# Kernel optimization log

Hardware: AMD Instinct MI355X
Metric: run time of the kernel (lower is better)

## Reference

```python
import jax, jax.numpy as jnp
import numpy as np

BS, N1, N2, D = 2, 512, 512, 64  # in_dim = out_dim = D
TEMP = 1.0
EPS = 1e-5
POOL_RATIO = 0.5


def setup_inputs() -> dict:
    key = jax.random.key(0)
    ks = iter(jax.random.split(key, 32))
    nrm = lambda shape, s=0.05: jax.random.normal(next(ks), shape, dtype=jnp.float32) * s
    inp = {
        "x1": jax.random.normal(next(ks), (BS, N1, D), dtype=jnp.float32),
        "x2": jax.random.normal(next(ks), (BS, N2, D), dtype=jnp.float32),
        # proj_type1 / proj_type2 (Linear in->in); weights stored [in, out]
        "W1": nrm((D, D)), "b1": jnp.zeros((D,), jnp.float32),
        "W2": nrm((D, D)), "b2": jnp.zeros((D,), jnp.float32),
        # att_proj / att_projM (Linear in->out)
        "Wa": nrm((D, D)), "ba": jnp.zeros((D,), jnp.float32),
        "WaM": nrm((D, D)), "baM": jnp.zeros((D,), jnp.float32),
        # attention weight vectors (out_dim, 1)
        "w11": nrm((D, 1), 0.2), "w22": nrm((D, 1), 0.2),
        "w12": nrm((D, 1), 0.2), "wM": nrm((D, 1), 0.2),
        # projections
        "Wpa": nrm((D, D)), "bpa": jnp.zeros((D,), jnp.float32),
        "Wwoa": nrm((D, D)), "bwoa": jnp.zeros((D,), jnp.float32),
        "WpaM": nrm((D, D)), "bpaM": jnp.zeros((D,), jnp.float32),
        "WwoaM": nrm((D, D)), "bwoaM": jnp.zeros((D,), jnp.float32),
        # BatchNorm1d affine params
        "gamma": jnp.ones((D,), jnp.float32), "beta": jnp.zeros((D,), jnp.float32),
        # GraphPool score layer (Linear D->1), shared pool as in Model
        "Wp": nrm((D, 1), 0.2), "bp": jnp.zeros((1,), jnp.float32),
    }
    return inp


def _htrg_gat(x1, x2, W1, b1, W2, b2, Wa, ba, WaM, baM, w11, w22, w12, wM,
              Wpa, bpa, Wwoa, bwoa, WpaM, bpaM, WwoaM, bwoaM, gamma, beta):
    n1 = x1.shape[1]
    x1p = x1 @ W1 + b1
    x2p = x2 @ W2 + b2
    x = jnp.concatenate([x1p, x2p], axis=1)          # (b, N, d)
    master = jnp.mean(x, axis=1, keepdims=True)       # (b, 1, d)

    # --- attention map: pairwise node products, blockwise score weights ---
    pair = x[:, :, None, :] * x[:, None, :, :]        # (b, N, N, d)
    t = jnp.tanh(pair @ Wa + ba)                      # (b, N, N, d)
    top = jnp.concatenate([t[:, :n1, :n1] @ w11, t[:, :n1, n1:] @ w12], axis=2)
    bot = jnp.concatenate([t[:, n1:, :n1] @ w12, t[:, n1:, n1:] @ w22], axis=2)
    board = jnp.concatenate([top, bot], axis=1) / TEMP  # (b, N, N, 1)
    att = jax.nn.softmax(board, axis=-2)

    # --- master update ---
    tm = jnp.tanh((x * master) @ WaM + baM)           # (b, N, d)
    am = jax.nn.softmax((tm @ wM) / TEMP, axis=-2)    # (b, N, 1)
    agg_m = jnp.einsum('bn,bnd->bd', am[..., 0], x)[:, None, :]  # (b, 1, d)
    master_new = (agg_m @ WpaM + bpaM) + (master @ WwoaM + bwoaM)

    # --- project nodes with attention ---
    agg = jnp.einsum('bij,bjd->bid', att[..., 0], x)  # (b, N, d)
    xo = (agg @ Wpa + bpa) + (x @ Wwoa + bwoa)

    # --- BatchNorm1d over flattened (b*N) rows, then SELU ---
    mu = jnp.mean(xo, axis=(0, 1))
    var = jnp.var(xo, axis=(0, 1))
    xo = (xo - mu) * jax.lax.rsqrt(var + EPS) * gamma + beta
    xo = jax.nn.selu(xo)
    return xo[:, :n1], xo[:, n1:], master_new


def _graph_pool(x, Wp, bp):
    # scores -> sigmoid -> scale features -> top-k gather
    n = x.shape[1]
    k = max(int(n * POOL_RATIO), 1)
    scores = jax.nn.sigmoid(x @ Wp + bp)              # (b, n, 1)
    _, idx = jax.lax.top_k(scores[..., 0], k)         # (b, k)
    xs = x * scores
    return jnp.take_along_axis(xs, idx[..., None], axis=1)  # (b, k, d)


def reference(x1, x2, W1, b1, W2, b2, Wa, ba, WaM, baM, w11, w22, w12, wM,
              Wpa, bpa, Wwoa, bwoa, WpaM, bpaM, WwoaM, bwoaM, gamma, beta, Wp, bp):
    o1, o2, master = _htrg_gat(x1, x2, W1, b1, W2, b2, Wa, ba, WaM, baM,
                               w11, w22, w12, wM, Wpa, bpa, Wwoa, bwoa,
                               WpaM, bpaM, WwoaM, bwoaM, gamma, beta)
    p1 = _graph_pool(o1, Wp, bp)
    p2 = _graph_pool(o2, Wp, bp)
    return jnp.concatenate([p1, p2], axis=1)          # (b, n1/2 + n2/2, d)
```

## Files before the change

### kernel.cpp

```cpp
#include <hip/hip_runtime.h>

typedef float f32x4 __attribute__((ext_vector_type(4)));
typedef short short8 __attribute__((ext_vector_type(8)));

#define N_TOT 1024
#define N_HALF 512
#define D 64
#define KPOOL 256

#if __has_builtin(__builtin_amdgcn_exp2f)
#define EXP2F(x) __builtin_amdgcn_exp2f(x)
#else
#define EXP2F(x) __expf((x) * 0.6931471805599453f)
#endif
#if __has_builtin(__builtin_amdgcn_rcpf)
#define RCPF(x) __builtin_amdgcn_rcpf(x)
#else
#define RCPF(x) (1.0f / (x))
#endif

__device__ __forceinline__ short f2bf(float v) {
    unsigned u = __float_as_uint(v);
    u += 0x7FFFu + ((u >> 16) & 1u);
    return (short)(u >> 16);
}
__device__ __forceinline__ float bf2f(unsigned short u) {
    return __uint_as_float(((unsigned)u) << 16);
}

__global__ void k_proj(const float* __restrict__ x1, const float* __restrict__ x2,
                       const float* __restrict__ W1, const float* __restrict__ b1,
                       const float* __restrict__ W2, const float* __restrict__ b2,
                       float* __restrict__ x_f, unsigned short* __restrict__ x_bf,
                       unsigned short* __restrict__ xT_hi, unsigned short* __restrict__ xT_lo) {
    int r = blockIdx.x;
    int b = r >> 10, n = r & 1023;
    const float *src, *W, *bias;
    if (n < N_HALF) { src = x1 + (b * N_HALF + n) * D;            W = W1; bias = b1; }
    else            { src = x2 + (b * N_HALF + (n - N_HALF)) * D; W = W2; bias = b2; }
    __shared__ float row[D];
    int t = threadIdx.x;
    row[t] = src[t];
    __syncthreads();
    float acc = bias[t];
#pragma unroll
    for (int d = 0; d < D; ++d) acc = fmaf(row[d], W[d * D + t], acc);
    unsigned short hi = (unsigned short)f2bf(acc);
    unsigned short lo = (unsigned short)f2bf(acc - bf2f(hi));
    x_f[r * D + t] = acc;
    x_bf[r * D + t] = hi;
    xT_hi[((size_t)b * D + t) * N_TOT + n] = hi;
    xT_lo[((size_t)b * D + t) * N_TOT + n] = lo;
}

__global__ void __launch_bounds__(256)
k_score(const float* __restrict__ x_f, const unsigned short* __restrict__ x_bf,
        const float* __restrict__ Wa, const float* __restrict__ ba,
        const float* __restrict__ w11, const float* __restrict__ w22,
        const float* __restrict__ w12,
        unsigned short* __restrict__ Ehi, unsigned short* __restrict__ Elo) {
    int bid = blockIdx.x;
    int b = (bid >= 2560) ? 1 : 0;
    int m = bid - b * 2560;
    int i, c0;
    if (m < 1024)      { i = m >> 2;                        c0 = m & 3; }
    else if (m < 1792) { int t = m - 1024; i = 256 + t / 3; c0 = t % 3; }
    else if (m < 2304) { int t = m - 1792; i = 512 + (t >> 1); c0 = t & 1; }
    else               { i = 768 + (m - 2304);              c0 = 0; }
    int jt0 = i >> 4;
    int jts = jt0 + (c0 << 4);
    int jte = (jts + 16 < 64) ? (jts + 16) : 64;

    int tid = threadIdx.x;
    int l = tid & 63, wv = tid >> 6;
    int kc = l & 15, dg = l >> 4;

    __shared__ float xi_s[D];
    if (tid < D) xi_s[tid] = x_f[(b * N_TOT + i) * D + tid];
    __syncthreads();

    const float C2 = 2.885390081777927f;
    const float LOG2E = 1.4426950408889634f;

    const float* wTop = (i < N_HALF) ? w11 : w12;
    const float* wBot = (i < N_HALF) ? w12 : w22;

    short8 bfrag[4][2];
    float bac[4], wm2A[4], wm2B[4];
    float wsumA = 0.f, wsumB = 0.f;
#pragma unroll
    for (int kt = 0; kt < 4; ++kt) {
        int kcol = kt * 16 + kc;
        bac[kt] = ba[kcol] * C2;
        float wA = wTop[kcol], wB = wBot[kcol];
        wm2A[kt] = -2.f * wA; wm2B[kt] = -2.f * wB;
        wsumA += wA; wsumB += wB;
#pragma unroll
        for (int mm = 0; mm < 2; ++mm) {
            short8 f;
#pragma unroll
            for (int e = 0; e < 8; ++e) {
                int d = mm * 32 + dg * 8 + e;
                f[e] = f2bf(xi_s[d] * Wa[d * D + kcol]);
            }
            bfrag[kt][mm] = f;
        }
    }

    const unsigned short* xb_b = x_bf + b * N_TOT * D;
    unsigned short* EbH = Ehi + ((size_t)b << 20);
    unsigned short* EbL = Elo + ((size_t)b << 20);
    for (int jt = jts + wv; jt < jte; jt += 4) {
        const unsigned short* arow = xb_b + (jt * 16 + kc) * D + dg * 8;
        short8 a0 = *reinterpret_cast<const short8*>(arow);
        short8 a1 = *reinterpret_cast<const short8*>(arow + 32);
        f32x4 acc[4];
#pragma unroll
        for (int kt = 0; kt < 4; ++kt) {
            f32x4 z = {0.f, 0.f, 0.f, 0.f};
            z = __builtin_amdgcn_mfma_f32_16x16x32_bf16(a0, bfrag[kt][0], z, 0, 0, 0);
            z = __builtin_amdgcn_mfma_f32_16x16x32_bf16(a1, bfrag[kt][1], z, 0, 0, 0);
            acc[kt] = z;
        }
        bool top = (jt < 32);
        float wsum_t = top ? wsumA : wsumB;
#pragma unroll
        for (int r = 0; r < 4; ++r) {
            float part = wsum_t;
#pragma unroll
            for (int kt = 0; kt < 4; ++kt) {
                float e2 = EXP2F(fmaf(acc[kt][r], C2, bac[kt]));
                float rcv = RCPF(e2 + 1.f);
                part = fmaf(top ? wm2A[kt] : wm2B[kt], rcv, part);
            }
            part += __shfl_xor(part, 1);
            part += __shfl_xor(part, 2);
            part += __shfl_xor(part, 4);
            part += __shfl_xor(part, 8);
            if (kc == 0) {
                int j = jt * 16 + dg * 4 + r;
                if (j >= i) {
                    float e = EXP2F(part * LOG2E);
                    unsigned short eh = (unsigned short)f2bf(e);
                    unsigned short el = (unsigned short)f2bf(e - bf2f(eh));
                    EbH[(size_t)i * N_TOT + j] = eh;
                    EbL[(size_t)i * N_TOT + j] = el;
                    if (j > i) {
                        EbH[(size_t)j * N_TOT + i] = eh;
                        EbL[(size_t)j * N_TOT + i] = el;
                    }
                }
            }
        }
    }
}

__global__ void __launch_bounds__(256)
k_agg(const unsigned short* __restrict__ Ehi, const unsigned short* __restrict__ Elo,
      const unsigned short* __restrict__ xT_hi, const unsigned short* __restrict__ xT_lo,
      const float* __restrict__ x_f,
      const float* __restrict__ Wpa, const float* __restrict__ bpa,
      const float* __restrict__ Wwoa, const float* __restrict__ bwoa,
      float* __restrict__ xo_pre, float* __restrict__ partials) {
    int b = blockIdx.x >> 6, it = blockIdx.x & 63;
    int i0 = it * 16;
    int tid = threadIdx.x;
    int l = tid & 63, wv = tid >> 6;
    int kc = l & 15, dg = l >> 4;

    const unsigned short* EbH = Ehi + ((size_t)b << 20);
    const unsigned short* EbL = Elo + ((size_t)b << 20);
    const unsigned short* xTH = xT_hi + (size_t)b * D * N_TOT;
    const unsigned short* xTL = xT_lo + (size_t)b * D * N_TOT;

    f32x4 C0 = {0.f, 0.f, 0.f, 0.f}, C1 = C0, C2v = C0;
    const unsigned short* AH = EbH + (size_t)(i0 + kc) * N_TOT + dg * 8;
    const unsigned short* AL = EbL + (size_t)(i0 + kc) * N_TOT + dg * 8;
    const unsigned short* BH = xTH + (size_t)(wv * 16 + kc) * N_TOT + dg * 8;
    const unsigned short* BL = xTL + (size_t)(wv * 16 + kc) * N_TOT + dg * 8;
#pragma unroll 4
    for (int ks = 0; ks < 32; ++ks) {
        short8 ah = *reinterpret_cast<const short8*>(AH + ks * 32);
        short8 bh = *reinterpret_cast<const short8*>(BH + ks * 32);
        C0 = __builtin_amdgcn_mfma_f32_16x16x32_bf16(ah, bh, C0, 0, 0, 0);
        short8 bl = *reinterpret_cast<const short8*>(BL + ks * 32);
        C1 = __builtin_amdgcn_mfma_f32_16x16x32_bf16(ah, bl, C1, 0, 0, 0);
        short8 al = *reinterpret_cast<const short8*>(AL + ks * 32);
        C2v = __builtin_amdgcn_mfma_f32_16x16x32_bf16(al, bh, C2v, 0, 0, 0);
    }
    f32x4 C = (C0 + C1) + C2v;

    __shared__ float aggL[16][D];
    __shared__ float xiL[16][D];
    __shared__ float xoL[16][D];
    __shared__ float rs_part[4][16];
    __shared__ float riL[16];

    {
        int row = l & 15, seg = l >> 4;
        size_t base = (size_t)(i0 + row) * N_TOT + wv * 256 + seg * 64;
        const unsigned short* ErH = EbH + base;
        const unsigned short* ErL = EbL + base;
        float rs = 0.f;
#pragma unroll
        for (int u = 0; u < 8; ++u) {
            short8 vh = *reinterpret_cast<const short8*>(ErH + u * 8);
            short8 vl = *reinterpret_cast<const short8*>(ErL + u * 8);
#pragma unroll
            for (int e = 0; e < 8; ++e)
                rs += bf2f((unsigned short)vh[e]) + bf2f((unsigned short)vl[e]);
        }
        rs += __shfl_xor(rs, 16);
        rs += __shfl_xor(rs, 32);
        if (l < 16) rs_part[wv][l] = rs;
    }

#pragma unroll
    for (int r = 0; r < 4; ++r)
        aggL[dg * 4 + r][wv * 16 + kc] = C[r];

    {
        int row = tid >> 4, quad = tid & 15;
        const f32x4* xf4 = reinterpret_cast<const f32x4*>(x_f + ((size_t)b * N_TOT + i0) * D);
        reinterpret_cast<f32x4*>(xiL)[row * 16 + quad] = xf4[row * 16 + quad];
    }
    __syncthreads();
    if (tid < 16)
        riL[tid] = 1.f / (rs_part[0][tid] + rs_part[1][tid] + rs_part[2][tid] + rs_part[3][tid]);
    __syncthreads();
#pragma unroll
    for (int u = 0; u < 4; ++u) {
        int idx = tid + 256 * u;
        reinterpret_cast<float*>(aggL)[idx] *= riL[idx >> 6];
    }
    __syncthreads();

    int k = l;
    float xo[4];
#pragma unroll
    for (int r = 0; r < 4; ++r) xo[r] = bpa[k] + bwoa[k];
    for (int dd = 0; dd < D; ++dd) {
        float wp = Wpa[dd * D + k], ww = Wwoa[dd * D + k];
#pragma unroll
        for (int r = 0; r < 4; ++r) {
            int row = wv * 4 + r;
            xo[r] += aggL[row][dd] * wp + xiL[row][dd] * ww;
        }
    }
#pragma unroll
    for (int r = 0; r < 4; ++r) {
        int row = wv * 4 + r;
        xo_pre[((size_t)b * N_TOT + i0 + row) * D + k] = xo[r];
        xoL[row][k] = xo[r];
    }
    __syncthreads();
    if (tid < D) {
        float s = 0.f, q = 0.f;
#pragma unroll
        for (int mm = 0; mm < 16; ++mm) { float v = xoL[mm][tid]; s += v; q = fmaf(v, v, q); }
        partials[blockIdx.x * 128 + tid] = s;
        partials[blockIdx.x * 128 + 64 + tid] = q;
    }
}

__global__ void k_stats2(const float* __restrict__ partials, float* __restrict__ stats) {
    int t = threadIdx.x;
    int g = t >> 7;
    int f128 = t & 127;
    float s = 0.f;
    for (int blk = g * 32; blk < g * 32 + 32; ++blk) s += partials[blk * 128 + f128];
    __shared__ float SQ[4][128];
    SQ[g][f128] = s;
    __syncthreads();
    if (t < 128) {
        float tot = SQ[0][t] + SQ[1][t] + SQ[2][t] + SQ[3][t];
        SQ[0][t] = tot;
    }
    __syncthreads();
    if (t < D) {
        float mu = SQ[0][t] * (1.f / 2048.f);
        float ex2 = SQ[0][64 + t] * (1.f / 2048.f);
        stats[t] = mu;
        stats[D + t] = rsqrtf(ex2 - mu * mu + 1e-5f);
    }
}

__global__ void k_norm(const float* __restrict__ xo_pre, const float* __restrict__ stats,
                       const float* __restrict__ gamma, const float* __restrict__ beta,
                       const float* __restrict__ Wp, const float* __restrict__ bp,
                       float* __restrict__ o_norm, float* __restrict__ scores) {
    int r = blockIdx.x * 4 + (threadIdx.x >> 6);
    int t = threadIdx.x & 63;
    float v = xo_pre[r * D + t];
    v = (v - stats[t]) * stats[D + t] * gamma[t] + beta[t];
    const float kScale = 1.0507009873554805f, kAlpha = 1.6732632423543772f;
    v = (v > 0.f) ? kScale * v : kScale * kAlpha * expm1f(v);
    o_norm[r * D + t] = v;
    float pd = v * Wp[t];
#pragma unroll
    for (int off = 32; off >= 1; off >>= 1) pd += __shfl_xor(pd, off);
    if (t == 0) scores[r] = 1.f / (1.f + __expf(-(pd + bp[0])));
}

__global__ void __launch_bounds__(512)
k_pool(const float* __restrict__ o_norm, const float* __restrict__ scores,
       float* __restrict__ out) {
    int b = blockIdx.x >> 1, half = blockIdx.x & 1;
    int tid = threadIdx.x;
    __shared__ float sc_s[N_HALF];
    __shared__ unsigned long long keys[N_HALF];
    __shared__ unsigned short map[KPOOL];

    {
        float sc = scores[b * N_TOT + half * N_HALF + tid];
        sc_s[tid] = sc;
        keys[tid] = ((unsigned long long)__float_as_uint(sc) << 10) | (unsigned)(511 - tid);
    }
    __syncthreads();
    unsigned long long mine = keys[tid];
    int cnt = 0;
#pragma unroll 8
    for (int qq = 0; qq < N_HALF; ++qq) cnt += (keys[qq] > mine) ? 1 : 0;
    if (cnt < KPOOL) map[cnt] = (unsigned short)tid;
    __syncthreads();
    int d = tid & 63;
    for (int rr = tid >> 6; rr < KPOOL; rr += 8) {
        int src = map[rr];
        out[(size_t)(b * N_HALF + half * KPOOL + rr) * D + d] =
            o_norm[(size_t)(b * N_TOT + half * N_HALF + src) * D + d] * sc_s[src];
    }
}

extern "C" void kernel_launch(void* const* d_in, const int* in_sizes, int n_in,
                              void* d_out, int out_size, void* d_ws, size_t ws_size,
                              hipStream_t stream) {
    const float* x1   = (const float*)d_in[0];
    const float* x2   = (const float*)d_in[1];
    const float* W1   = (const float*)d_in[2];
    const float* b1   = (const float*)d_in[3];
    const float* W2   = (const float*)d_in[4];
    const float* b2   = (const float*)d_in[5];
    const float* Wa   = (const float*)d_in[6];
    const float* ba   = (const float*)d_in[7];
    const float* w11  = (const float*)d_in[10];
    const float* w22  = (const float*)d_in[11];
    const float* w12  = (const float*)d_in[12];
    const float* Wpa  = (const float*)d_in[14];
    const float* bpa  = (const float*)d_in[15];
    const float* Wwoa = (const float*)d_in[16];
    const float* bwoa = (const float*)d_in[17];
    const float* gamma= (const float*)d_in[22];
    const float* beta = (const float*)d_in[23];
    const float* Wp   = (const float*)d_in[24];
    const float* bp   = (const float*)d_in[25];
    float* out = (float*)d_out;

    char* ws = (char*)d_ws;
    float*          x_f     = (float*)(ws + 0);
    unsigned short* x_bf    = (unsigned short*)(ws + 524288);
    unsigned short* xT_hi   = (unsigned short*)(ws + 786432);
    unsigned short* xT_lo   = (unsigned short*)(ws + 1048576);
    unsigned short* Ehi     = (unsigned short*)(ws + 1310720);
    unsigned short* Elo     = (unsigned short*)(ws + 5505024);
    float*          xo_pre  = (float*)(ws + 9699328);
    float*          o_norm  = (float*)(ws + 10223616);
    float*          scores  = (float*)(ws + 10747904);
    float*          partials= (float*)(ws + 10756096);
    float*          stats   = (float*)(ws + 10821632);

    hipLaunchKernelGGL(k_proj, dim3(2 * N_TOT), dim3(64), 0, stream,
                       x1, x2, W1, b1, W2, b2, x_f, x_bf, xT_hi, xT_lo);
    hipLaunchKernelGGL(k_score, dim3(5120), dim3(256), 0, stream,
                       x_f, x_bf, Wa, ba, w11, w22, w12, Ehi, Elo);
    hipLaunchKernelGGL(k_agg, dim3(128), dim3(256), 0, stream,
                       Ehi, Elo, xT_hi, xT_lo, x_f, Wpa, bpa, Wwoa, bwoa, xo_pre, partials);
    hipLaunchKernelGGL(k_stats2, dim3(1), dim3(512), 0, stream, partials, stats);
    hipLaunchKernelGGL(k_norm, dim3(512), dim3(256), 0, stream,
                       xo_pre, stats, gamma, beta, Wp, bp, o_norm, scores);
    hipLaunchKernelGGL(k_pool, dim3(4), dim3(512), 0, stream, o_norm, scores, out);
}
```

Before: 103.5 us.

## Split aggregation over key quarters and stage transposed Wa for score kernel

The aggregation kernel, previously 128 blocks each doing the full 1024-long reduction, is split into 512 blocks that each handle a quarter of the key dimension. They write partial aggregates and row sums, and a new finalize kernel reduces them and applies the output projections and BN partial statistics. The change is meant to fix poor GPU occupancy in the aggregation stage. It costs an extra kernel launch and a round trip of partial results through global memory. Separately, Wa is transposed once in an extra k_proj block so that k_score can load weights and bias/score vectors as vectors or through shared memory instead of strided scalar global loads.

```diff
diff --git a/kernel.cpp b/kernel.cpp
--- a/kernel.cpp
+++ b/kernel.cpp
@@ -31,15 +31,20 @@
 __global__ void k_proj(const float* __restrict__ x1, const float* __restrict__ x2,
                        const float* __restrict__ W1, const float* __restrict__ b1,
                        const float* __restrict__ W2, const float* __restrict__ b2,
+                       const float* __restrict__ Wa, float* __restrict__ WaT_f,
                        float* __restrict__ x_f, unsigned short* __restrict__ x_bf,
                        unsigned short* __restrict__ xT_hi, unsigned short* __restrict__ xT_lo) {
+    int t = threadIdx.x;
+    if (blockIdx.x == 2048) {
+        for (int k = 0; k < D; ++k) WaT_f[k * D + t] = Wa[t * D + k];
+        return;
+    }
     int r = blockIdx.x;
     int b = r >> 10, n = r & 1023;
     const float *src, *W, *bias;
     if (n < N_HALF) { src = x1 + (b * N_HALF + n) * D;            W = W1; bias = b1; }
     else            { src = x2 + (b * N_HALF + (n - N_HALF)) * D; W = W2; bias = b2; }
     __shared__ float row[D];
-    int t = threadIdx.x;
     row[t] = src[t];
     __syncthreads();
     float acc = bias[t];
@@ -55,7 +60,7 @@
 
 __global__ void __launch_bounds__(256)
 k_score(const float* __restrict__ x_f, const unsigned short* __restrict__ x_bf,
-        const float* __restrict__ Wa, const float* __restrict__ ba,
+        const float* __restrict__ WaT_f, const float* __restrict__ ba,
         const float* __restrict__ w11, const float* __restrict__ w22,
         const float* __restrict__ w12,
         unsigned short* __restrict__ Ehi, unsigned short* __restrict__ Elo) {
@@ -75,34 +80,42 @@
     int l = tid & 63, wv = tid >> 6;
     int kc = l & 15, dg = l >> 4;
 
-    __shared__ float xi_s[D];
-    if (tid < D) xi_s[tid] = x_f[(b * N_TOT + i) * D + tid];
-    __syncthreads();
-
     const float C2 = 2.885390081777927f;
     const float LOG2E = 1.4426950408889634f;
 
     const float* wTop = (i < N_HALF) ? w11 : w12;
     const float* wBot = (i < N_HALF) ? w12 : w22;
+
+    __shared__ float xi_s[D];
+    __shared__ float ba_s[D], wA_s[D], wB_s[D];
+    if (tid < D) xi_s[tid] = x_f[(b * N_TOT + i) * D + tid];
+    else if (tid < 2 * D) ba_s[tid - D] = ba[tid - D] * C2;
+    else if (tid < 3 * D) wA_s[tid - 2 * D] = wTop[tid - 2 * D];
+    else                  wB_s[tid - 3 * D] = wBot[tid - 3 * D];
+    __syncthreads();
 
     short8 bfrag[4][2];
     float bac[4], wm2A[4], wm2B[4];
     float wsumA = 0.f, wsumB = 0.f;
+    const f32x4* xi4 = reinterpret_cast<const f32x4*>(xi_s);
 #pragma unroll
     for (int kt = 0; kt < 4; ++kt) {
         int kcol = kt * 16 + kc;
-        bac[kt] = ba[kcol] * C2;
-        float wA = wTop[kcol], wB = wBot[kcol];
+        bac[kt] = ba_s[kcol];
+        float wA = wA_s[kcol], wB = wB_s[kcol];
         wm2A[kt] = -2.f * wA; wm2B[kt] = -2.f * wB;
         wsumA += wA; wsumB += wB;
+        const float* wrow = WaT_f + kcol * D;
 #pragma unroll
         for (int mm = 0; mm < 2; ++mm) {
+            const f32x4* wp = reinterpret_cast<const f32x4*>(wrow + mm * 32 + dg * 8);
+            f32x4 w0 = wp[0], w1 = wp[1];
+            f32x4 xa = xi4[mm * 8 + dg * 2], xb = xi4[mm * 8 + dg * 2 + 1];
             short8 f;
 #pragma unroll
-            for (int e = 0; e < 8; ++e) {
-                int d = mm * 32 + dg * 8 + e;
-                f[e] = f2bf(xi_s[d] * Wa[d * D + kcol]);
-            }
+            for (int e = 0; e < 4; ++e) f[e] = f2bf(xa[e] * w0[e]);
+#pragma unroll
+            for (int e = 0; e < 4; ++e) f[e + 4] = f2bf(xb[e] * w1[e]);
             bfrag[kt][mm] = f;
         }
     }
@@ -156,14 +169,13 @@
 }
 
 __global__ void __launch_bounds__(256)
-k_agg(const unsigned short* __restrict__ Ehi, const unsigned short* __restrict__ Elo,
-      const unsigned short* __restrict__ xT_hi, const unsigned short* __restrict__ xT_lo,
-      const float* __restrict__ x_f,
-      const float* __restrict__ Wpa, const float* __restrict__ bpa,
-      const float* __restrict__ Wwoa, const float* __restrict__ bwoa,
-      float* __restrict__ xo_pre, float* __restrict__ partials) {
-    int b = blockIdx.x >> 6, it = blockIdx.x & 63;
-    int i0 = it * 16;
+k_aggp(const unsigned short* __restrict__ Ehi, const unsigned short* __restrict__ Elo,
+       const unsigned short* __restrict__ xT_hi, const unsigned short* __restrict__ xT_lo,
+       float* __restrict__ pagg, float* __restrict__ rowsum_part) {
+    int blk = blockIdx.x;
+    int b = blk >> 8, rest = blk & 255;
+    int it = rest >> 2, q = rest & 3;
+    int i0 = it * 16, jbase = q * 256;
     int tid = threadIdx.x;
     int l = tid & 63, wv = tid >> 6;
     int kc = l & 15, dg = l >> 4;
@@ -174,12 +186,12 @@
     const unsigned short* xTL = xT_lo + (size_t)b * D * N_TOT;
 
     f32x4 C0 = {0.f, 0.f, 0.f, 0.f}, C1 = C0, C2v = C0;
-    const unsigned short* AH = EbH + (size_t)(i0 + kc) * N_TOT + dg * 8;
-    const unsigned short* AL = EbL + (size_t)(i0 + kc) * N_TOT + dg * 8;
-    const unsigned short* BH = xTH + (size_t)(wv * 16 + kc) * N_TOT + dg * 8;
-    const unsigned short* BL = xTL + (size_t)(wv * 16 + kc) * N_TOT + dg * 8;
-#pragma unroll 4
-    for (int ks = 0; ks < 32; ++ks) {
+    const unsigned short* AH = EbH + (size_t)(i0 + kc) * N_TOT + jbase + dg * 8;
+    const unsigned short* AL = EbL + (size_t)(i0 + kc) * N_TOT + jbase + dg * 8;
+    const unsigned short* BH = xTH + (size_t)(wv * 16 + kc) * N_TOT + jbase + dg * 8;
+    const unsigned short* BL = xTL + (size_t)(wv * 16 + kc) * N_TOT + jbase + dg * 8;
+#pragma unroll
+    for (int ks = 0; ks < 8; ++ks) {
         short8 ah = *reinterpret_cast<const short8*>(AH + ks * 32);
         short8 bh = *reinterpret_cast<const short8*>(BH + ks * 32);
         C0 = __builtin_amdgcn_mfma_f32_16x16x32_bf16(ah, bh, C0, 0, 0, 0);
@@ -190,76 +202,70 @@
     }
     f32x4 C = (C0 + C1) + C2v;
 
-    __shared__ float aggL[16][D];
-    __shared__ float xiL[16][D];
-    __shared__ float xoL[16][D];
-    __shared__ float rs_part[4][16];
-    __shared__ float riL[16];
-
     {
-        int row = l & 15, seg = l >> 4;
-        size_t base = (size_t)(i0 + row) * N_TOT + wv * 256 + seg * 64;
-        const unsigned short* ErH = EbH + base;
-        const unsigned short* ErL = EbL + base;
+        int row = wv * 4 + (l & 3);
+        int seg = l >> 2;
+        size_t base = (size_t)(i0 + row) * N_TOT + jbase + seg * 16;
         float rs = 0.f;
 #pragma unroll
-        for (int u = 0; u < 8; ++u) {
-            short8 vh = *reinterpret_cast<const short8*>(ErH + u * 8);
-            short8 vl = *reinterpret_cast<const short8*>(ErL + u * 8);
+        for (int u = 0; u < 2; ++u) {
+            short8 vh = *reinterpret_cast<const short8*>(EbH + base + u * 8);
+            short8 vl = *reinterpret_cast<const short8*>(EbL + base + u * 8);
 #pragma unroll
             for (int e = 0; e < 8; ++e)
                 rs += bf2f((unsigned short)vh[e]) + bf2f((unsigned short)vl[e]);
         }
+        rs += __shfl_xor(rs, 4);
+        rs += __shfl_xor(rs, 8);
         rs += __shfl_xor(rs, 16);
         rs += __shfl_xor(rs, 32);
-        if (l < 16) rs_part[wv][l] = rs;
+        if (l < 4) rowsum_part[(size_t)(b * 4 + q) * N_TOT + i0 + wv * 4 + l] = rs;
     }
 
 #pragma unroll
     for (int r = 0; r < 4; ++r)
-        aggL[dg * 4 + r][wv * 16 + kc] = C[r];
-
-    {
-        int row = tid >> 4, quad = tid & 15;
-        const f32x4* xf4 = reinterpret_cast<const f32x4*>(x_f + ((size_t)b * N_TOT + i0) * D);
-        reinterpret_cast<f32x4*>(xiL)[row * 16 + quad] = xf4[row * 16 + quad];
-    }
-    __syncthreads();
-    if (tid < 16)
-        riL[tid] = 1.f / (rs_part[0][tid] + rs_part[1][tid] + rs_part[2][tid] + rs_part[3][tid]);
-    __syncthreads();
-#pragma unroll
-    for (int u = 0; u < 4; ++u) {
-        int idx = tid + 256 * u;
-        reinterpret_cast<float*>(aggL)[idx] *= riL[idx >> 6];
-    }
-    __syncthreads();
-
-    int k = l;
-    float xo[4];
-#pragma unroll
-    for (int r = 0; r < 4; ++r) xo[r] = bpa[k] + bwoa[k];
-    for (int dd = 0; dd < D; ++dd) {
-        float wp = Wpa[dd * D + k], ww = Wwoa[dd * D + k];
-#pragma unroll
-        for (int r = 0; r < 4; ++r) {
-            int row = wv * 4 + r;
-            xo[r] += aggL[row][dd] * wp + xiL[row][dd] * ww;
-        }
-    }
-#pragma unroll
-    for (int r = 0; r < 4; ++r) {
-        int row = wv * 4 + r;
-        xo_pre[((size_t)b * N_TOT + i0 + row) * D + k] = xo[r];
-        xoL[row][k] = xo[r];
-    }
-    __syncthreads();
-    if (tid < D) {
-        float s = 0.f, q = 0.f;
-#pragma unroll
-        for (int mm = 0; mm < 16; ++mm) { float v = xoL[mm][tid]; s += v; q = fmaf(v, v, q); }
-        partials[blockIdx.x * 128 + tid] = s;
-        partials[blockIdx.x * 128 + 64 + tid] = q;
+        pagg[((size_t)(b * 4 + q) * N_TOT + i0 + dg * 4 + r) * D + wv * 16 + kc] = C[r];
+}
+
+__global__ void __launch_bounds__(256)
+k_aggfin(const float* __restrict__ pagg, const float* __restrict__ rowsum_part,
+         const float* __restrict__ x_f,
+         const float* __restrict__ Wpa, const float* __restrict__ bpa,
+         const float* __restrict__ Wwoa, const float* __restrict__ bwoa,
+         float* __restrict__ xo_pre, float* __restrict__ partials) {
+    int tid = threadIdx.x;
+    int rl = tid >> 6, k = tid & 63;
+    int r = blockIdx.x * 4 + rl;
+    int b = r >> 10, i = r & 1023;
+
+    float rs = 0.f, a = 0.f;
+#pragma unroll
+    for (int jc = 0; jc < 4; ++jc) {
+        rs += rowsum_part[(size_t)(b * 4 + jc) * N_TOT + i];
+        a  += pagg[((size_t)(b * 4 + jc) * N_TOT + i) * D + k];
+    }
+    float ri = 1.f / rs;
+
+    __shared__ float aggL[4][D];
+    __shared__ float xiL[4][D];
+    aggL[rl][k] = a * ri;
+    xiL[rl][k] = x_f[(size_t)r * D + k];
+    __syncthreads();
+    float xo = bpa[k] + bwoa[k];
+#pragma unroll 8
+    for (int dd = 0; dd < D; ++dd)
+        xo += aggL[rl][dd] * Wpa[dd * D + k] + xiL[rl][dd] * Wwoa[dd * D + k];
+    xo_pre[(size_t)r * D + k] = xo;
+
+    __syncthreads();
+    aggL[rl][k] = xo;
+    xiL[rl][k] = xo * xo;
+    __syncthreads();
+    if (rl == 0) {
+        float s = aggL[0][k] + aggL[1][k] + aggL[2][k] + aggL[3][k];
+        float qs = xiL[0][k] + xiL[1][k] + xiL[2][k] + xiL[3][k];
+        partials[blockIdx.x * 128 + k] = s;
+        partials[blockIdx.x * 128 + 64 + k] = qs;
     }
 }
 
@@ -268,7 +274,7 @@
     int g = t >> 7;
     int f128 = t & 127;
     float s = 0.f;
-    for (int blk = g * 32; blk < g * 32 + 32; ++blk) s += partials[blk * 128 + f128];
+    for (int blk = g * 128; blk < g * 128 + 128; ++blk) s += partials[blk * 128 + f128];
     __shared__ float SQ[4][128];
     SQ[g][f128] = s;
     __syncthreads();
@@ -362,18 +368,23 @@
     unsigned short* xT_lo   = (unsigned short*)(ws + 1048576);
     unsigned short* Ehi     = (unsigned short*)(ws + 1310720);
     unsigned short* Elo     = (unsigned short*)(ws + 5505024);
-    float*          xo_pre  = (float*)(ws + 9699328);
-    float*          o_norm  = (float*)(ws + 10223616);
-    float*          scores  = (float*)(ws + 10747904);
-    float*          partials= (float*)(ws + 10756096);
-    float*          stats   = (float*)(ws + 10821632);
-
-    hipLaunchKernelGGL(k_proj, dim3(2 * N_TOT), dim3(64), 0, stream,
-                       x1, x2, W1, b1, W2, b2, x_f, x_bf, xT_hi, xT_lo);
+    float*          WaT_f   = (float*)(ws + 9699328);
+    float*          pagg    = (float*)(ws + 9715712);
+    float*          rowsum  = (float*)(ws + 11812864);
+    float*          xo_pre  = (float*)(ws + 11845632);
+    float*          o_norm  = (float*)(ws + 12369920);
+    float*          scores  = (float*)(ws + 12894208);
+    float*          partials= (float*)(ws + 12902400);
+    float*          stats   = (float*)(ws + 13164544);
+
+    hipLaunchKernelGGL(k_proj, dim3(2 * N_TOT + 1), dim3(64), 0, stream,
+                       x1, x2, W1, b1, W2, b2, Wa, WaT_f, x_f, x_bf, xT_hi, xT_lo);
     hipLaunchKernelGGL(k_score, dim3(5120), dim3(256), 0, stream,
-                       x_f, x_bf, Wa, ba, w11, w22, w12, Ehi, Elo);
-    hipLaunchKernelGGL(k_agg, dim3(128), dim3(256), 0, stream,
-                       Ehi, Elo, xT_hi, xT_lo, x_f, Wpa, bpa, Wwoa, bwoa, xo_pre, partials);
+                       x_f, x_bf, WaT_f, ba, w11, w22, w12, Ehi, Elo);
+    hipLaunchKernelGGL(k_aggp, dim3(512), dim3(256), 0, stream,
+                       Ehi, Elo, xT_hi, xT_lo, pagg, rowsum);
+    hipLaunchKernelGGL(k_aggfin, dim3(512), dim3(256), 0, stream,
+                       pagg, rowsum, x_f, Wpa, bpa, Wwoa, bwoa, xo_pre, partials);
     hipLaunchKernelGGL(k_stats2, dim3(1), dim3(512), 0, stream, partials, stats);
     hipLaunchKernelGGL(k_norm, dim3(512), dim3(256), 0, stream,
                        xo_pre, stats, gamma, beta, Wp, bp, o_norm, scores);
```

Measured after the change: 144.5 us. 1.4x slower.

## Pack hi/lo attention weights and split aggregation over key halves

Applied to the files above, without the earlier changes.

Stores the hi and lo bf16 halves of each attention weight packed into one 32-bit word, so the score kernel issues one store per element instead of two and the aggregation reads one stream. The aggregation kernel is split into a partial kernel over two halves of the key dimension, doubling the grid from 128 to 256 blocks, and a finalize kernel that sums the partials and applies the projections. This adds an extra launch and an fp32 partial-buffer round trip in exchange for more parallelism in the memory-bound reduction.

```diff
diff --git a/kernel.cpp b/kernel.cpp
--- a/kernel.cpp
+++ b/kernel.cpp
@@ -57,8 +57,7 @@
 k_score(const float* __restrict__ x_f, const unsigned short* __restrict__ x_bf,
         const float* __restrict__ Wa, const float* __restrict__ ba,
         const float* __restrict__ w11, const float* __restrict__ w22,
-        const float* __restrict__ w12,
-        unsigned short* __restrict__ Ehi, unsigned short* __restrict__ Elo) {
+        const float* __restrict__ w12, unsigned* __restrict__ Ep) {
     int bid = blockIdx.x;
     int b = (bid >= 2560) ? 1 : 0;
     int m = bid - b * 2560;
@@ -108,8 +107,7 @@
     }
 
     const unsigned short* xb_b = x_bf + b * N_TOT * D;
-    unsigned short* EbH = Ehi + ((size_t)b << 20);
-    unsigned short* EbL = Elo + ((size_t)b << 20);
+    unsigned* Eb = Ep + ((size_t)b << 20);
     for (int jt = jts + wv; jt < jte; jt += 4) {
         const unsigned short* arow = xb_b + (jt * 16 + kc) * D + dg * 8;
         short8 a0 = *reinterpret_cast<const short8*>(arow);
@@ -143,12 +141,9 @@
                     float e = EXP2F(part * LOG2E);
                     unsigned short eh = (unsigned short)f2bf(e);
                     unsigned short el = (unsigned short)f2bf(e - bf2f(eh));
-                    EbH[(size_t)i * N_TOT + j] = eh;
-                    EbL[(size_t)i * N_TOT + j] = el;
-                    if (j > i) {
-                        EbH[(size_t)j * N_TOT + i] = eh;
-                        EbL[(size_t)j * N_TOT + i] = el;
-                    }
+                    unsigned pk = ((unsigned)eh << 16) | (unsigned)el;
+                    Eb[(size_t)i * N_TOT + j] = pk;
+                    if (j > i) Eb[(size_t)j * N_TOT + i] = pk;
                 }
             }
         }
@@ -156,81 +151,105 @@
 }
 
 __global__ void __launch_bounds__(256)
-k_agg(const unsigned short* __restrict__ Ehi, const unsigned short* __restrict__ Elo,
-      const unsigned short* __restrict__ xT_hi, const unsigned short* __restrict__ xT_lo,
-      const float* __restrict__ x_f,
-      const float* __restrict__ Wpa, const float* __restrict__ bpa,
-      const float* __restrict__ Wwoa, const float* __restrict__ bwoa,
-      float* __restrict__ xo_pre, float* __restrict__ partials) {
+k_aggp(const unsigned* __restrict__ Ep,
+       const unsigned short* __restrict__ xT_hi, const unsigned short* __restrict__ xT_lo,
+       float* __restrict__ pagg, float* __restrict__ rowsum_part) {
+    int blk = blockIdx.x;
+    int b = blk >> 7, rest = blk & 127;
+    int it = rest >> 1, jh = rest & 1;
+    int i0 = it * 16, jbase = jh * 512;
+    int tid = threadIdx.x;
+    int l = tid & 63, wv = tid >> 6;
+    int kc = l & 15, dg = l >> 4;
+
+    const unsigned* Eb = Ep + ((size_t)b << 20);
+    const unsigned short* xTH = xT_hi + (size_t)b * D * N_TOT;
+    const unsigned short* xTL = xT_lo + (size_t)b * D * N_TOT;
+
+    f32x4 C0 = {0.f, 0.f, 0.f, 0.f}, C1 = C0, C2v = C0;
+    const unsigned* Ap = Eb + (size_t)(i0 + kc) * N_TOT + jbase + dg * 8;
+    const unsigned short* BH = xTH + (size_t)(wv * 16 + kc) * N_TOT + jbase + dg * 8;
+    const unsigned short* BL = xTL + (size_t)(wv * 16 + kc) * N_TOT + jbase + dg * 8;
+#pragma unroll 4
+    for (int ks = 0; ks < 16; ++ks) {
+        uint4 p0 = *reinterpret_cast<const uint4*>(Ap + ks * 32);
+        uint4 p1 = *reinterpret_cast<const uint4*>(Ap + ks * 32 + 4);
+        short8 ah, al;
+        ah[0] = (short)(p0.x >> 16); al[0] = (short)(p0.x & 0xffff);
+        ah[1] = (short)(p0.y >> 16); al[1] = (short)(p0.y & 0xffff);
+        ah[2] = (short)(p0.z >> 16); al[2] = (short)(p0.z & 0xffff);
+        ah[3] = (short)(p0.w >> 16); al[3] = (short)(p0.w & 0xffff);
+        ah[4] = (short)(p1.x >> 16); al[4] = (short)(p1.x & 0xffff);
+        ah[5] = (short)(p1.y >> 16); al[5] = (short)(p1.y & 0xffff);
+        ah[6] = (short)(p1.z >> 16); al[6] = (short)(p1.z & 0xffff);
+        ah[7] = (short)(p1.w >> 16); al[7] = (short)(p1.w & 0xffff);
+        short8 bh = *reinterpret_cast<const short8*>(BH + ks * 32);
+        short8 bl = *reinterpret_cast<const short8*>(BL + ks * 32);
+        C0 = __builtin_amdgcn_mfma_f32_16x16x32_bf16(ah, bh, C0, 0, 0, 0);
+        C1 = __builtin_amdgcn_mfma_f32_16x16x32_bf16(ah, bl, C1, 0, 0, 0);
+        C2v = __builtin_amdgcn_mfma_f32_16x16x32_bf16(al, bh, C2v, 0, 0, 0);
+    }
+    f32x4 C = (C0 + C1) + C2v;
+
+    {
+        int row = wv * 4 + (l & 3);
+        int seg = l >> 2;
+        const unsigned* Er = Eb + (size_t)(i0 + row) * N_TOT + jbase + seg * 32;
+        float rs = 0.f;
+#pragma unroll
+        for (int u = 0; u < 8; ++u) {
+            uint4 v = *reinterpret_cast<const uint4*>(Er + u * 4);
+            rs += __uint_as_float(v.x & 0xffff0000u) + __uint_as_float(v.x << 16);
+            rs += __uint_as_float(v.y & 0xffff0000u) + __uint_as_float(v.y << 16);
+            rs += __uint_as_float(v.z & 0xffff0000u) + __uint_as_float(v.z << 16);
+            rs += __uint_as_float(v.w & 0xffff0000u) + __uint_as_float(v.w << 16);
+        }
+        rs += __shfl_xor(rs, 4);
+        rs += __shfl_xor(rs, 8);
+        rs += __shfl_xor(rs, 16);
+        rs += __shfl_xor(rs, 32);
+        if ((l & 3) == (l >> 2) % 4 && l < 4)
+            ;
+        if (l < 4) rowsum_part[(size_t)(b * 2 + jh) * N_TOT + i0 + wv * 4 + l] = rs;
+    }
+
+#pragma unroll
+    for (int r = 0; r < 4; ++r)
+        pagg[((size_t)(b * 2 + jh) * N_TOT + i0 + dg * 4 + r) * D + wv * 16 + kc] = C[r];
+}
+
+__global__ void __launch_bounds__(256)
+k_aggfin(const float* __restrict__ pagg, const float* __restrict__ rowsum_part,
+         const float* __restrict__ x_f,
+         const float* __restrict__ Wpa, const float* __restrict__ bpa,
+         const float* __restrict__ Wwoa, const float* __restrict__ bwoa,
+         float* __restrict__ xo_pre, float* __restrict__ partials) {
     int b = blockIdx.x >> 6, it = blockIdx.x & 63;
     int i0 = it * 16;
     int tid = threadIdx.x;
     int l = tid & 63, wv = tid >> 6;
-    int kc = l & 15, dg = l >> 4;
-
-    const unsigned short* EbH = Ehi + ((size_t)b << 20);
-    const unsigned short* EbL = Elo + ((size_t)b << 20);
-    const unsigned short* xTH = xT_hi + (size_t)b * D * N_TOT;
-    const unsigned short* xTL = xT_lo + (size_t)b * D * N_TOT;
-
-    f32x4 C0 = {0.f, 0.f, 0.f, 0.f}, C1 = C0, C2v = C0;
-    const unsigned short* AH = EbH + (size_t)(i0 + kc) * N_TOT + dg * 8;
-    const unsigned short* AL = EbL + (size_t)(i0 + kc) * N_TOT + dg * 8;
-    const unsigned short* BH = xTH + (size_t)(wv * 16 + kc) * N_TOT + dg * 8;
-    const unsigned short* BL = xTL + (size_t)(wv * 16 + kc) * N_TOT + dg * 8;
-#pragma unroll 4
-    for (int ks = 0; ks < 32; ++ks) {
-        short8 ah = *reinterpret_cast<const short8*>(AH + ks * 32);
-        short8 bh = *reinterpret_cast<const short8*>(BH + ks * 32);
-        C0 = __builtin_amdgcn_mfma_f32_16x16x32_bf16(ah, bh, C0, 0, 0, 0);
-        short8 bl = *reinterpret_cast<const short8*>(BL + ks * 32);
-        C1 = __builtin_amdgcn_mfma_f32_16x16x32_bf16(ah, bl, C1, 0, 0, 0);
-        short8 al = *reinterpret_cast<const short8*>(AL + ks * 32);
-        C2v = __builtin_amdgcn_mfma_f32_16x16x32_bf16(al, bh, C2v, 0, 0, 0);
-    }
-    f32x4 C = (C0 + C1) + C2v;
 
     __shared__ float aggL[16][D];
     __shared__ float xiL[16][D];
     __shared__ float xoL[16][D];
-    __shared__ float rs_part[4][16];
     __shared__ float riL[16];
 
-    {
-        int row = l & 15, seg = l >> 4;
-        size_t base = (size_t)(i0 + row) * N_TOT + wv * 256 + seg * 64;
-        const unsigned short* ErH = EbH + base;
-        const unsigned short* ErL = EbL + base;
-        float rs = 0.f;
-#pragma unroll
-        for (int u = 0; u < 8; ++u) {
-            short8 vh = *reinterpret_cast<const short8*>(ErH + u * 8);
-            short8 vl = *reinterpret_cast<const short8*>(ErL + u * 8);
-#pragma unroll
-            for (int e = 0; e < 8; ++e)
-                rs += bf2f((unsigned short)vh[e]) + bf2f((unsigned short)vl[e]);
-        }
-        rs += __shfl_xor(rs, 16);
-        rs += __shfl_xor(rs, 32);
-        if (l < 16) rs_part[wv][l] = rs;
-    }
-
-#pragma unroll
-    for (int r = 0; r < 4; ++r)
-        aggL[dg * 4 + r][wv * 16 + kc] = C[r];
-
-    {
-        int row = tid >> 4, quad = tid & 15;
-        const f32x4* xf4 = reinterpret_cast<const f32x4*>(x_f + ((size_t)b * N_TOT + i0) * D);
-        reinterpret_cast<f32x4*>(xiL)[row * 16 + quad] = xf4[row * 16 + quad];
-    }
-    __syncthreads();
+    const float* p0 = pagg + ((size_t)(b * 2 + 0) * N_TOT + i0) * D;
+    const float* p1 = pagg + ((size_t)(b * 2 + 1) * N_TOT + i0) * D;
+    const float* xB = x_f + ((size_t)b * N_TOT + i0) * D;
+#pragma unroll
+    for (int u = 0; u < 4; ++u) {
+        int idx = tid + u * 256;
+        reinterpret_cast<float*>(aggL)[idx] = p0[idx] + p1[idx];
+        reinterpret_cast<float*>(xiL)[idx] = xB[idx];
+    }
     if (tid < 16)
-        riL[tid] = 1.f / (rs_part[0][tid] + rs_part[1][tid] + rs_part[2][tid] + rs_part[3][tid]);
+        riL[tid] = 1.f / (rowsum_part[(size_t)(b * 2 + 0) * N_TOT + i0 + tid] +
+                          rowsum_part[(size_t)(b * 2 + 1) * N_TOT + i0 + tid]);
     __syncthreads();
 #pragma unroll
     for (int u = 0; u < 4; ++u) {
-        int idx = tid + 256 * u;
+        int idx = tid + u * 256;
         reinterpret_cast<float*>(aggL)[idx] *= riL[idx >> 6];
     }
     __syncthreads();
@@ -360,20 +379,23 @@
     unsigned short* x_bf    = (unsigned short*)(ws + 524288);
     unsigned short* xT_hi   = (unsigned short*)(ws + 786432);
     unsigned short* xT_lo   = (unsigned short*)(ws + 1048576);
-    unsigned short* Ehi     = (unsigned short*)(ws + 1310720);
-    unsigned short* Elo     = (unsigned short*)(ws + 5505024);
-    float*          xo_pre  = (float*)(ws + 9699328);
-    float*          o_norm  = (float*)(ws + 10223616);
-    float*          scores  = (float*)(ws + 10747904);
-    float*          partials= (float*)(ws + 10756096);
-    float*          stats   = (float*)(ws + 10821632);
+    unsigned*       Ep      = (unsigned*)(ws + 1310720);
+    float*          pagg    = (float*)(ws + 9699328);
+    float*          rowsum  = (float*)(ws + 10747904);
+    float*          xo_pre  = (float*)(ws + 10764288);
+    float*          o_norm  = (float*)(ws + 11288576);
+    float*          scores  = (float*)(ws + 11812864);
+    float*          partials= (float*)(ws + 11821056);
+    float*          stats   = (float*)(ws + 11886592);
 
     hipLaunchKernelGGL(k_proj, dim3(2 * N_TOT), dim3(64), 0, stream,
                        x1, x2, W1, b1, W2, b2, x_f, x_bf, xT_hi, xT_lo);
     hipLaunchKernelGGL(k_score, dim3(5120), dim3(256), 0, stream,
-                       x_f, x_bf, Wa, ba, w11, w22, w12, Ehi, Elo);
-    hipLaunchKernelGGL(k_agg, dim3(128), dim3(256), 0, stream,
-                       Ehi, Elo, xT_hi, xT_lo, x_f, Wpa, bpa, Wwoa, bwoa, xo_pre, partials);
+                       x_f, x_bf, Wa, ba, w11, w22, w12, Ep);
+    hipLaunchKernelGGL(k_aggp, dim3(256), dim3(256), 0, stream,
+                       Ep, xT_hi, xT_lo, pagg, rowsum);
+    hipLaunchKernelGGL(k_aggfin, dim3(128), dim3(256), 0, stream,
+                       pagg, rowsum, x_f, Wpa, bpa, Wwoa, bwoa, xo_pre, partials);
     hipLaunchKernelGGL(k_stats2, dim3(1), dim3(512), 0, stream, partials, stats);
     hipLaunchKernelGGL(k_norm, dim3(512), dim3(256), 0, stream,
                        xo_pre, stats, gamma, beta, Wp, bp, o_norm, scores);
```

After: 91.18 us. -11.9%, faster.
